# Optimization experiments

Hardware: AMD Instinct MI355X
Metric: run time of the kernel (lower is better)

Reference implementation:

```python
import jax, jax.numpy as jnp
import numpy as np

T, B, X, H = 512, 32, 1024, 1024


def setup_inputs() -> dict:
    key = jax.random.key(0)
    ks = jax.random.split(key, 12)
    n = lambda k, s: 0.1 * jax.random.normal(k, s, dtype=jnp.float32)
    return {
        "x": jax.random.normal(ks[0], (T, B, X), dtype=jnp.float32),
        "W_ix": n(ks[1], (X, H)), "W_ih": n(ks[2], (H, H)), "W_ic": n(ks[3], (H, H)),
        "W_fx": n(ks[4], (X, H)), "W_fh": n(ks[5], (H, H)), "W_fc": n(ks[6], (H, H)),
        "W_cx": n(ks[7], (X, H)), "W_ch": n(ks[8], (H, H)),
        "W_ox": n(ks[9], (X, H)), "W_oh": n(ks[10], (H, H)), "W_oc": n(ks[11], (H, H)),
        "b_i": jnp.zeros((H,), jnp.float32),
        "b_f": jnp.zeros((B, H), jnp.float32),  # faithful: per-batch forget bias
        "b_c": jnp.zeros((H,), jnp.float32),
        "b_o": jnp.zeros((H,), jnp.float32),
    }


def reference(x, W_ix, W_ih, W_ic, W_fx, W_fh, W_fc, W_cx, W_ch,
              W_ox, W_oh, W_oc, b_i, b_f, b_c, b_o):
    Bv, Hv = x.shape[1], W_ih.shape[0]

    # Precompute all input-side projections in one batched GEMM pass: [T,B,4H]
    Wx = jnp.concatenate([W_ix, W_fx, W_cx, W_ox], axis=1)
    xg = jnp.einsum('tbx,xg->tbg', x, Wx)
    xi, xf, xc, xo = jnp.split(xg, 4, axis=-1)

    def step(carry, xs):
        h_1, c_1 = carry
        xi_t, xf_t, xc_t, xo_t = xs
        i = jax.nn.sigmoid(xi_t + h_1 @ W_ih + c_1 @ W_ic + b_i)
        f = jax.nn.sigmoid(xf_t + h_1 @ W_fh + c_1 @ W_fc + b_f)
        c = f * c_1 + i * jnp.tanh(xc_t + h_1 @ W_ch + b_c)
        o = jax.nn.sigmoid(xo_t + h_1 @ W_oh + c @ W_oc + b_o)
        h = o * jnp.tanh(c)
        return (h, c), None

    h0 = jnp.zeros((Bv, Hv), x.dtype)
    c0 = jnp.zeros((Bv, Hv), x.dtype)
    (h, c), _ = jax.lax.scan(step, (h0, c0), (xi, xf, xc, xo))
    return h
```

## Files before the change

### kernel.cpp

```cpp
#include <hip/hip_runtime.h>
#include <hip/hip_bf16.h>
#include <stdint.h>

typedef unsigned short u16;
typedef uint32_t u32;
typedef unsigned long long u64;
typedef float f32x4 __attribute__((ext_vector_type(4)));
typedef __bf16 bf16x8 __attribute__((ext_vector_type(8)));

__device__ inline u16 f2bf(float f) {
  __bf16 h = (__bf16)f;
  return __builtin_bit_cast(u16, h);
}
__device__ inline f32x4 mfma16(bf16x8 a, bf16x8 b, f32x4 c) {
  return __builtin_amdgcn_mfma_f32_16x16x32_bf16(a, b, c, 0, 0, 0);
}
__device__ inline void cvt8(const float* p, bf16x8& h, bf16x8& l) {
  f32x4 u = *(const f32x4*)p;
  f32x4 v = *(const f32x4*)(p + 4);
#pragma unroll
  for (int i = 0; i < 4; ++i) {
    float a = u[i]; __bf16 ah = (__bf16)a; h[i] = ah; l[i] = (__bf16)(a - (float)ah);
    float b = v[i]; __bf16 bh = (__bf16)b; h[i + 4] = bh; l[i + 4] = (__bf16)(b - (float)bh);
  }
}
__device__ inline void gather8(const float* p, bf16x8& h, bf16x8& l) {
#pragma unroll
  for (int e = 0; e < 8; ++e) {
    float f = p[(size_t)e * 1024];
    __bf16 x = (__bf16)f;
    h[e] = x; l[e] = (__bf16)(f - (float)x);
  }
}

__device__ inline u64 ld64(const u64* p) {
  return __hip_atomic_load(p, __ATOMIC_RELAXED, __HIP_MEMORY_SCOPE_AGENT);
}
__device__ inline u32 ld32(const u32* p) {
  return __hip_atomic_load(p, __ATOMIC_RELAXED, __HIP_MEMORY_SCOPE_AGENT);
}
__device__ inline void st32(u32* p, u32 v) {
  __hip_atomic_store(p, v, __ATOMIC_RELAXED, __HIP_MEMORY_SCOPE_AGENT);
}

struct B16Pair { u64 a, b; };
__device__ inline bf16x8 ldfrag(const u64* base, int j8, int row) {
  B16Pair p;
  p.a = ld64(base + (j8 << 6) + row);
  p.b = ld64(base + (j8 << 6) + 32 + row);
  return __builtin_bit_cast(bf16x8, p);
}

struct RecArgs {
  const float* x;
  const float *W_ix, *W_ih, *W_ic, *W_fx, *W_fh, *W_fc, *W_cx, *W_ch;
  const float *W_ox, *W_oh, *W_oc;
  const float *b_i, *b_f, *b_c, *b_o;
  u32 *hB, *cB;
  u32* flags;
  u32* done;
  float* out;
};

__device__ inline void arriveT(u32* flags, unsigned ep, int wg) {
  __syncthreads();
  if (threadIdx.x == 0) st32(flags + wg, ep);
}
__device__ inline void waitT(u32* flags, u32* done, unsigned ep, int wg) {
  const int tid = threadIdx.x;
  if (wg == 0) {
    const int wv = tid >> 6, ln = tid & 63;
    if (wv < 4) {
      int it = 0;
      for (;;) {
        u32 v = ld32(flags + wv * 64 + ln);
        if (__ballot(v >= ep) == ~0ull) break;
        if (++it > 400000) break;
        __builtin_amdgcn_s_sleep(1);
      }
    }
    __syncthreads();
    if (tid < 16) st32(done + tid * 16, ep);
  } else if (tid == 0) {
    const u32* dp = done + (wg & 15) * 16;
    int it = 0;
    while (ld32(dp) < ep && it < 400000) {
      __builtin_amdgcn_s_sleep(1);
      ++it;
    }
  }
  __syncthreads();
}

__global__ __launch_bounds__(512, 1) void lstm_rec(RecArgs a) {
  __shared__ float scr[8 * 2 * 16 * 17];

  const int tid = threadIdx.x;
  const int wg = blockIdx.x;
  const int j0 = wg * 4;
  const int lane = tid & 63;
  const int wave = tid >> 6;
  const int mrow = lane & 15;
  const int kgroup = lane >> 4;
  const int kq = kgroup * 8;
  const int kw = wave * 128;
  const int col = lane & 15;
  const int rq = (lane >> 4) * 4;

  const u64* H64 = (const u64*)a.hB;
  const u64* C64 = (const u64*)a.cB;

  const int fjj = col >> 2, fg = col & 3;
  const int fj = j0 + fjj;
  const float* Wx = (fg == 0) ? a.W_ix : (fg == 1) ? a.W_fx : (fg == 2) ? a.W_cx : a.W_ox;
  const float* Wh = (fg == 0) ? a.W_ih : (fg == 1) ? a.W_fh : (fg == 2) ? a.W_ch : a.W_oh;
  const float* Wc = (fg == 0) ? a.W_ic : (fg == 1) ? a.W_fc : (fg == 3) ? a.W_oc : a.W_ic;

  bf16x8 bxh[4], bxl[4], bhh[4], bhl[4], bch[4], bcl[4];
#pragma unroll
  for (int ks = 0; ks < 4; ++ks) {
    const size_t k8 = (size_t)(kw + ks * 32 + kq);
    gather8(Wx + k8 * 1024 + fj, bxh[ks], bxl[ks]);
    gather8(Wh + k8 * 1024 + fj, bhh[ks], bhl[ks]);
    if (fg != 2) {
      gather8(Wc + k8 * 1024 + fj, bch[ks], bcl[ks]);
    } else {
      bf16x8 z = {};
      bch[ks] = z; bcl[ks] = z;
    }
  }

  const int eb = tid >> 2, ejj = tid & 3, ej = j0 + (tid & 3);
  const u32 swidx = ((u32)(ej >> 3) << 7) | ((u32)((ej >> 2) & 1) << 6)
                  | ((u32)eb << 1) | ((u32)(ej >> 1) & 1);
  if (tid < 128 && (tid & 1) == 0) {
    st32(a.hB + swidx, 0u);
    st32(a.cB + swidx, 0u);
  }
  float bi = 0.f, bfv = 0.f, bcv = 0.f, bo = 0.f;
  if (tid < 128) {
    bi = a.b_i[ej]; bfv = a.b_f[eb * 1024 + ej]; bcv = a.b_c[ej]; bo = a.b_o[ej];
  }

  unsigned ep = 0;
  arriveT(a.flags, ++ep, wg);
  bf16x8 xph0[4], xpl0[4], xph1[4], xpl1[4];
#pragma unroll
  for (int ks = 0; ks < 4; ++ks) {
    const float* xp = a.x + ((size_t)mrow << 10) + kw + ks * 32 + kq;
    cvt8(xp, xph0[ks], xpl0[ks]);
    cvt8(xp + (16 << 10), xph1[ks], xpl1[ks]);
  }
  waitT(a.flags, a.done, ep, wg);

  float c_reg = 0.f, o_pre = 0.f;
  bf16x8 cf0[4] = {}, cf1[4] = {};
  f32x4 pc0 = {}, pc1 = {};
#pragma unroll
  for (int ks = 0; ks < 4; ++ks) {
    pc0 = mfma16(cf0[ks], bch[ks], pc0);
    pc0 = mfma16(cf0[ks], bcl[ks], pc0);
    pc1 = mfma16(cf1[ks], bch[ks], pc1);
    pc1 = mfma16(cf1[ks], bcl[ks], pc1);
  }

  for (int t = 0; t < 512; ++t) {
    f32x4 acc0 = {}, acc1 = {};
#pragma unroll
    for (int ks = 0; ks < 4; ++ks) {
      const int j8 = wave * 16 + ks * 4 + kgroup;
      bf16x8 ah0 = ldfrag(H64, j8, mrow);
      bf16x8 ah1 = ldfrag(H64, j8, mrow + 16);
      acc0 = mfma16(xph0[ks], bxh[ks], acc0);
      acc0 = mfma16(xpl0[ks], bxh[ks], acc0);
      acc0 = mfma16(xph0[ks], bxl[ks], acc0);
      acc0 = mfma16(ah0, bhh[ks], acc0);
      acc0 = mfma16(ah0, bhl[ks], acc0);
      acc1 = mfma16(xph1[ks], bxh[ks], acc1);
      acc1 = mfma16(xpl1[ks], bxh[ks], acc1);
      acc1 = mfma16(xph1[ks], bxl[ks], acc1);
      acc1 = mfma16(ah1, bhh[ks], acc1);
      acc1 = mfma16(ah1, bhl[ks], acc1);
    }
    {
      const bool take_pc = (col & 3) != 3;
#pragma unroll
      for (int v = 0; v < 4; ++v) {
        scr[((wave * 2 + 0) * 16 + rq + v) * 17 + col] = acc0[v] + (take_pc ? pc0[v] : 0.f);
        scr[((wave * 2 + 1) * 16 + rq + v) * 17 + col] = acc1[v] + (take_pc ? pc1[v] : 0.f);
      }
    }
    __syncthreads();
    if (tid < 128) {
      float pre[4];
#pragma unroll
      for (int g = 0; g < 4; ++g) {
        float s = 0.f;
#pragma unroll
        for (int w = 0; w < 8; ++w)
          s += scr[((w * 2 + (eb >> 4)) * 16 + (eb & 15)) * 17 + ejj * 4 + g];
        pre[g] = s;
      }
      float iv = 1.f / (1.f + expf(-(pre[0] + bi)));
      float fv = 1.f / (1.f + expf(-(pre[1] + bfv)));
      float cv = tanhf(pre[2] + bcv);
      c_reg = fv * c_reg + iv * cv;
      u32 cb = (u32)f2bf(c_reg);
      u32 cpart = __shfl_xor(cb, 1);
      if ((tid & 1) == 0) st32(a.cB + swidx, cb | (cpart << 16));
      o_pre = pre[3] + bo;
    }
    arriveT(a.flags, ++ep, wg);
    {
      const int tn = (t < 511) ? t + 1 : 511;
#pragma unroll
      for (int ks = 0; ks < 4; ++ks) {
        const float* xp = a.x + ((size_t)(tn * 32 + mrow) << 10) + kw + ks * 32 + kq;
        cvt8(xp, xph0[ks], xpl0[ks]);
        cvt8(xp + (16 << 10), xph1[ks], xpl1[ks]);
      }
    }
    waitT(a.flags, a.done, ep, wg);

    f32x4 a20 = {}, a21 = {};
#pragma unroll
    for (int ks = 0; ks < 4; ++ks) {
      const int j8 = wave * 16 + ks * 4 + kgroup;
      cf0[ks] = ldfrag(C64, j8, mrow);
      cf1[ks] = ldfrag(C64, j8, mrow + 16);
      a20 = mfma16(cf0[ks], bch[ks], a20);
      a20 = mfma16(cf0[ks], bcl[ks], a20);
      a21 = mfma16(cf1[ks], bch[ks], a21);
      a21 = mfma16(cf1[ks], bcl[ks], a21);
    }
#pragma unroll
    for (int v = 0; v < 4; ++v) {
      scr[((wave * 2 + 0) * 16 + rq + v) * 17 + col] = a20[v];
      scr[((wave * 2 + 1) * 16 + rq + v) * 17 + col] = a21[v];
    }
    __syncthreads();
    if (tid < 128) {
      float s = o_pre;
#pragma unroll
      for (int w = 0; w < 8; ++w)
        s += scr[((w * 2 + (eb >> 4)) * 16 + (eb & 15)) * 17 + ejj * 4 + 3];
      float ov = 1.f / (1.f + expf(-s));
      float hv = ov * tanhf(c_reg);
      u32 hb = (u32)f2bf(hv);
      u32 hpart = __shfl_xor(hb, 1);
      if ((tid & 1) == 0) st32(a.hB + swidx, hb | (hpart << 16));
      if (t == 511) a.out[eb * 1024 + ej] = hv;
    }
    arriveT(a.flags, ++ep, wg);
    {
      f32x4 npc0 = {}, npc1 = {};
#pragma unroll
      for (int ks = 0; ks < 4; ++ks) {
        npc0 = mfma16(cf0[ks], bch[ks], npc0);
        npc0 = mfma16(cf0[ks], bcl[ks], npc0);
        npc1 = mfma16(cf1[ks], bch[ks], npc1);
        npc1 = mfma16(cf1[ks], bcl[ks], npc1);
      }
      pc0 = npc0; pc1 = npc1;
    }
    waitT(a.flags, a.done, ep, wg);
  }
}

extern "C" void kernel_launch(void* const* d_in, const int* in_sizes, int n_in,
                              void* d_out, int out_size, void* d_ws, size_t ws_size,
                              hipStream_t stream) {
  (void)in_sizes; (void)n_in; (void)out_size;
  RecArgs ra;
  ra.x    = (const float*)d_in[0];
  ra.W_ix = (const float*)d_in[1];
  ra.W_ih = (const float*)d_in[2];
  ra.W_ic = (const float*)d_in[3];
  ra.W_fx = (const float*)d_in[4];
  ra.W_fh = (const float*)d_in[5];
  ra.W_fc = (const float*)d_in[6];
  ra.W_cx = (const float*)d_in[7];
  ra.W_ch = (const float*)d_in[8];
  ra.W_ox = (const float*)d_in[9];
  ra.W_oh = (const float*)d_in[10];
  ra.W_oc = (const float*)d_in[11];
  ra.b_i  = (const float*)d_in[12];
  ra.b_f  = (const float*)d_in[13];
  ra.b_c  = (const float*)d_in[14];
  ra.b_o  = (const float*)d_in[15];

  char* ws = (char*)d_ws;
  size_t off = 0;
  auto alloc = [&](size_t bytes) {
    char* p = ws + off;
    off = (off + bytes + 255) & ~(size_t)255;
    return p;
  };
  ra.hB    = (u32*)alloc(32 * 1024 * 2);
  ra.cB    = (u32*)alloc(32 * 1024 * 2);
  ra.flags = (u32*)alloc(1024);
  ra.done  = (u32*)alloc(16 * 64);
  ra.out   = (float*)d_out;
  if (off > ws_size) return;

  (void)hipMemsetAsync(ra.flags, 0, 1024, stream);
  (void)hipMemsetAsync(ra.done, 0, 16 * 64, stream);

  void* args[] = {&ra};
  hipError_t e = hipLaunchCooperativeKernel((void*)lstm_rec, dim3(256), dim3(512),
                                            args, 0, stream);
  if (e != hipSuccess) {
    lstm_rec<<<dim3(256), dim3(512), 0, stream>>>(ra);
  }
}
```

Baseline: 5.227 ms.

## Replace centralized grid barrier with all-to-all flag polling

The grid barrier used to have workgroup 0 gather all 256 arrival flags and then publish a done counter that the other workgroups polled. Now every workgroup polls all 256 flags itself, with one wave reading four flags per lane through two 64-bit loads. This removes one serial hop (gather, then broadcast) from each of the two barriers per timestep. In exchange, all workgroups now poll the same flag cache lines at once, which adds memory contention.

```diff
diff --git a/kernel.cpp b/kernel.cpp
--- a/kernel.cpp
+++ b/kernel.cpp
@@ -34,9 +34,6 @@
 }
 
 __device__ inline u64 ld64(const u64* p) {
-  return __hip_atomic_load(p, __ATOMIC_RELAXED, __HIP_MEMORY_SCOPE_AGENT);
-}
-__device__ inline u32 ld32(const u32* p) {
   return __hip_atomic_load(p, __ATOMIC_RELAXED, __HIP_MEMORY_SCOPE_AGENT);
 }
 __device__ inline void st32(u32* p, u32 v) {
@@ -58,7 +55,6 @@
   const float *b_i, *b_f, *b_c, *b_o;
   u32 *hB, *cB;
   u32* flags;
-  u32* done;
   float* out;
 };
 
@@ -66,27 +62,17 @@
   __syncthreads();
   if (threadIdx.x == 0) st32(flags + wg, ep);
 }
-__device__ inline void waitT(u32* flags, u32* done, unsigned ep, int wg) {
-  const int tid = threadIdx.x;
-  if (wg == 0) {
-    const int wv = tid >> 6, ln = tid & 63;
-    if (wv < 4) {
-      int it = 0;
-      for (;;) {
-        u32 v = ld32(flags + wv * 64 + ln);
-        if (__ballot(v >= ep) == ~0ull) break;
-        if (++it > 400000) break;
-        __builtin_amdgcn_s_sleep(1);
-      }
-    }
-    __syncthreads();
-    if (tid < 16) st32(done + tid * 16, ep);
-  } else if (tid == 0) {
-    const u32* dp = done + (wg & 15) * 16;
+__device__ inline void waitA(const u32* flags, unsigned ep) {
+  if (threadIdx.x < 64) {
+    const u64* f = (const u64*)flags + threadIdx.x * 2;
     int it = 0;
-    while (ld32(dp) < ep && it < 400000) {
+    for (;;) {
+      u64 q0 = ld64(f), q1 = ld64(f + 1);
+      bool ok = ((u32)q0 >= ep) & ((u32)(q0 >> 32) >= ep) &
+                ((u32)q1 >= ep) & ((u32)(q1 >> 32) >= ep);
+      if (__ballot(ok) == ~0ull) break;
+      if (++it > 400000) break;
       __builtin_amdgcn_s_sleep(1);
-      ++it;
     }
   }
   __syncthreads();
@@ -151,7 +137,7 @@
     cvt8(xp, xph0[ks], xpl0[ks]);
     cvt8(xp + (16 << 10), xph1[ks], xpl1[ks]);
   }
-  waitT(a.flags, a.done, ep, wg);
+  waitA(a.flags, ep);
 
   float c_reg = 0.f, o_pre = 0.f;
   bf16x8 cf0[4] = {}, cf1[4] = {};
@@ -220,7 +206,7 @@
         cvt8(xp + (16 << 10), xph1[ks], xpl1[ks]);
       }
     }
-    waitT(a.flags, a.done, ep, wg);
+    waitA(a.flags, ep);
 
     f32x4 a20 = {}, a21 = {};
 #pragma unroll
@@ -263,7 +249,7 @@
       }
       pc0 = npc0; pc1 = npc1;
     }
-    waitT(a.flags, a.done, ep, wg);
+    waitA(a.flags, ep);
   }
 }
 
@@ -299,12 +285,10 @@
   ra.hB    = (u32*)alloc(32 * 1024 * 2);
   ra.cB    = (u32*)alloc(32 * 1024 * 2);
   ra.flags = (u32*)alloc(1024);
-  ra.done  = (u32*)alloc(16 * 64);
   ra.out   = (float*)d_out;
   if (off > ws_size) return;
 
   (void)hipMemsetAsync(ra.flags, 0, 1024, stream);
-  (void)hipMemsetAsync(ra.done, 0, 16 * 64, stream);
 
   void* args[] = {&ra};
   hipError_t e = hipLaunchCooperativeKernel((void*)lstm_rec, dim3(256), dim3(512),
```

Result: faster. 5.057 ms (median of 2 runs) (-3.3%).
